# Kernel optimization log

Measured on AMD Instinct MI355X. Metric: run time of the kernel, lower is better.

Reference implementation:

```python
import jax, jax.numpy as jnp
import numpy as np

B, N, E = 8, 1024, 131072
DS, DT, D, HEADS = 768, 128, 256, 4
DH = D // HEADS  # 64, cross-attn head dim


def _gat(x, src, dst, lin_w, att_src, att_dst, bias, n):
    # PyG GATConv(heads=4, concat=False): per-head dim == out_channels == D
    xw = (x @ lin_w).reshape(n, HEADS, D)                  # [n,H,D]
    a_s = jnp.sum(xw * att_src, axis=-1)                   # [n,H]
    a_d = jnp.sum(xw * att_dst, axis=-1)                   # [n,H]
    alpha = jax.nn.leaky_relu(a_s[src] + a_d[dst], 0.2)    # [E',H]
    # softmax over incoming edges per destination node (self-loops guarantee non-empty segments)
    amax = jax.ops.segment_max(alpha, dst, num_segments=n)
    ex = jnp.exp(alpha - amax[dst])
    den = jax.ops.segment_sum(ex, dst, num_segments=n)
    w = ex / den[dst]                                      # [E',H]
    out = jax.ops.segment_sum(xw[src] * w[:, :, None], dst, num_segments=n)  # [n,H,D]
    return out.mean(axis=1) + bias                         # concat=False -> mean over heads


def _mha(q, kv, in_w, in_b, out_w, out_b):
    # torch nn.MultiheadAttention packed projections: in_w [3D,D], in_b [3D]
    qh = (q @ in_w[:D].T + in_b[:D]).reshape(B, N, HEADS, DH)
    kh = (kv @ in_w[D:2 * D].T + in_b[D:2 * D]).reshape(B, N, HEADS, DH)
    vh = (kv @ in_w[2 * D:].T + in_b[2 * D:]).reshape(B, N, HEADS, DH)
    s = jnp.einsum('bqhd,bkhd->bhqk', qh, kh) / np.float32(np.sqrt(DH))
    a = jax.nn.softmax(s, axis=-1)
    o = jnp.einsum('bhqk,bkhd->bqhd', a, vh).reshape(B, N, D)
    return o @ out_w.T + out_b


def _forward(structure_emb, text_emb, node_features, edit_emb_raw,
             ws, bs, wt, bt, we, be, wp, bp,
             g1_lin, g1_as, g1_ad, g1_b, g2_lin, g2_as, g2_ad, g2_b,
             mha_iw, mha_ib, mha_ow, mha_ob,
             cw1, cb1, cw2, cb2, aw1, ab1, aw2, ab2,
             edge_index, node_mask):
    maskf = node_mask.astype(jnp.float32)                  # [B,N]
    struct = structure_emb @ ws + bs                       # [B,N,D]
    textf = text_emb @ wt + bt                             # [B,D]
    editp = edit_emb_raw @ we + be                         # [B,D] (frozen-encoder CLS already precomputed)
    text_feat = jnp.broadcast_to(textf[:, None], (B, N, D))
    edit_feat = jnp.broadcast_to(editp[:, None], (B, N, D))
    combined = jnp.concatenate([struct, text_feat, edit_feat], axis=-1)  # [B,N,3D]
    node = (combined @ wp + bp) * maskf[..., None]
    x = node.reshape(B * N, D)
    edit_flat = edit_feat.reshape(B * N, D)
    n = B * N
    loops = jnp.arange(n, dtype=edge_index.dtype)          # GATConv default add_self_loops=True
    src = jnp.concatenate([edge_index[0], loops])
    dst = jnp.concatenate([edge_index[1], loops])
    x = jax.nn.relu(_gat(x + edit_flat, src, dst, g1_lin, g1_as, g1_ad, g1_b, n))
    x = jax.nn.relu(_gat(x + edit_flat, src, dst, g2_lin, g2_as, g2_ad, g2_b, n))
    node = x.reshape(B, N, D)
    # global attention over [text, edit] context tokens
    gte = jnp.stack([textf, editp], axis=1)                # [B,2,D]
    scores = jnp.einsum('bnd,bkd->bnk', node, gte) + (1.0 - maskf)[..., None] * -10000.0
    wglob = jax.nn.softmax(scores, axis=-1) @ gte          # [B,N,D]
    attn = _mha(node, text_feat, mha_iw, mha_ib, mha_ow, mha_ob)
    comb = node + wglob + attn
    coords = (jax.nn.relu(comb @ cw1 + cb1) @ cw2 + cb2) * maskf[..., None]   # [B,N,3]
    aa_logits = (jax.nn.relu(comb @ aw1 + ab1) @ aw2 + ab2) * maskf[..., None]  # [B,N,20]
    aa_probs = jax.nn.softmax(aa_logits, axis=-1) * maskf[..., None]
    return coords, aa_probs


def setup_inputs() -> dict:
    key = jax.random.key(0)
    ki = iter(jax.random.split(key, 48))
    def rn(shape, s=1.0):
        return jax.random.normal(next(ki), shape, jnp.float32) * s
    inp = {
        'structure_emb': rn((B, N, DS)),
        'text_emb': rn((B, DT)),
        'node_features': rn((B, N, D)),   # accepted by forward but unused (as in original)
        'edit_emb_raw': rn((B, DS)),
        'ws': rn((DS, D), 0.02), 'bs': rn((D,), 0.02),
        'wt': rn((DT, D), 0.02), 'bt': rn((D,), 0.02),
        'we': rn((DS, D), 0.02), 'be': rn((D,), 0.02),
        'wp': rn((3 * D, D), 0.02), 'bp': rn((D,), 0.02),
        'g1_lin': rn((D, HEADS * D), 0.02), 'g1_as': rn((HEADS, D), 0.02), 'g1_ad': rn((HEADS, D), 0.02), 'g1_b': rn((D,), 0.02),
        'g2_lin': rn((D, HEADS * D), 0.02), 'g2_as': rn((HEADS, D), 0.02), 'g2_ad': rn((HEADS, D), 0.02), 'g2_b': rn((D,), 0.02),
        'mha_iw': rn((3 * D, D), 0.02), 'mha_ib': rn((3 * D,), 0.02),
        'mha_ow': rn((D, D), 0.02), 'mha_ob': rn((D,), 0.02),
        'cw1': rn((D, D), 0.02), 'cb1': rn((D,), 0.02), 'cw2': rn((D, 3), 0.02), 'cb2': rn((3,), 0.02),
        'aw1': rn((D, D), 0.02), 'ab1': rn((D,), 0.02), 'aw2': rn((D, 20), 0.02), 'ab2': rn((20,), 0.02),
        'edge_index': jax.random.randint(next(ki), (2, E), 0, B * N, dtype=jnp.int32),
        'node_mask': jnp.ones((B, N), dtype=bool),
    }
    return inp


def reference(structure_emb, text_emb, node_features, edit_emb_raw,
              ws, bs, wt, bt, we, be, wp, bp,
              g1_lin, g1_as, g1_ad, g1_b, g2_lin, g2_as, g2_ad, g2_b,
              mha_iw, mha_ib, mha_ow, mha_ob,
              cw1, cb1, cw2, cb2, aw1, ab1, aw2, ab2,
              edge_index, node_mask):
    return _forward(structure_emb, text_emb, node_features, edit_emb_raw,
                    ws, bs, wt, bt, we, be, wp, bp,
                    g1_lin, g1_as, g1_ad, g1_b, g2_lin, g2_as, g2_ad, g2_b,
                    mha_iw, mha_ib, mha_ow, mha_ob,
                    cw1, cb1, cw2, cb2, aw1, ab1, aw2, ab2,
                    edge_index, node_mask)
```

## Files before the change

### kernel.cpp

```cpp
#include <hip/hip_runtime.h>
#include <hip/hip_bf16.h>

#define BB 8
#define NN 1024
#define BN 8192
#define DD 256
#define HEADS 4
#define HD 1024
#define DSS 768
#define DTT 128
#define NE 131072
#define NEP (NE + BN)
#define DEGCAP 256

typedef __hip_bfloat16 bf16;
typedef __attribute__((ext_vector_type(8))) short short8;
typedef __attribute__((ext_vector_type(4))) float floatx4;

__device__ __forceinline__ float toF(bf16 x){ return __bfloat162float(x); }
__device__ __forceinline__ void stC(float* p, float v){ *p = v; }
__device__ __forceinline__ void stC(bf16* p, float v){ *p = __float2bfloat16(v); }
__device__ __forceinline__ float bf_lo(unsigned u){ return __uint_as_float(u << 16); }
__device__ __forceinline__ float bf_hi(unsigned u){ return __uint_as_float(u & 0xffff0000u); }

__device__ __forceinline__ float wredsum(float v){
  #pragma unroll
  for (int off = 32; off; off >>= 1) v += __shfl_xor(v, off);
  return v;
}
__device__ __forceinline__ float wredmax(float v){
  #pragma unroll
  for (int off = 32; off; off >>= 1) v = fmaxf(v, __shfl_xor(v, off));
  return v;
}

__device__ __forceinline__ void dev_transpose(
    float tb[32][33], const float* __restrict__ src, bf16* __restrict__ dst,
    int R, int C, int bx, int by, int tid)
{
  int c0 = bx*32, r0 = by*32;
  int tr = tid >> 5, tc = tid & 31;
  #pragma unroll
  for (int i = 0; i < 4; i++)
    tb[tr + i*8][tc] = src[(size_t)(r0 + tr + i*8)*C + c0 + tc];
  __syncthreads();
  #pragma unroll
  for (int i = 0; i < 4; i++)
    dst[(size_t)(c0 + tr + i*8)*R + r0 + tc] = __float2bfloat16(tb[tc][tr + i*8]);
}

__global__ __launch_bounds__(256) void prep1(
    const float* __restrict__ text_emb, const float* __restrict__ edit_emb,
    const float* __restrict__ wt, const float* __restrict__ bt,
    const float* __restrict__ we, const float* __restrict__ be,
    float* __restrict__ textf, float* __restrict__ editp,
    const float* __restrict__ wsm, const float* __restrict__ wp, bf16* __restrict__ WfT,
    const float* __restrict__ semb, bf16* __restrict__ sembB,
    const float* __restrict__ g1_lin, bf16* __restrict__ g1T,
    const float* __restrict__ g2_lin, bf16* __restrict__ g2T,
    const float* __restrict__ cw1, const float* __restrict__ aw1, bf16* __restrict__ W2T,
    const float* __restrict__ cw2, const float* __restrict__ cb2,
    const float* __restrict__ aw2, const float* __restrict__ ab2,
    bf16* __restrict__ WdT, float* __restrict__ bias23,
    int* __restrict__ counts, int* __restrict__ fc, float* __restrict__ zz,
    const float* __restrict__ cb1, const float* __restrict__ ab1, float* __restrict__ bias2)
{
  __shared__ float tpose[32][33];
  __shared__ float red[2][4][64];
  int blk = blockIdx.x, tid = threadIdx.x;
  if (blk < 32) {
    int b = blk & 7, l = tid & 63, qq = tid >> 6;
    int d = (blk >> 3)*64 + l;
    float tf = 0.f;
    for (int k = qq*32; k < qq*32 + 32; k++) tf += text_emb[b*DTT + k] * wt[(size_t)k*DD + d];
    float ep = 0.f;
    for (int k = qq*192; k < qq*192 + 192; k++) ep += edit_emb[b*DSS + k] * we[(size_t)k*DD + d];
    red[0][qq][l] = tf; red[1][qq][l] = ep;
    __syncthreads();
    if (tid < 64) {
      int dd = (blk >> 3)*64 + tid;
      textf[b*DD + dd] = red[0][0][tid]+red[0][1][tid]+red[0][2][tid]+red[0][3][tid] + bt[dd];
      editp[b*DD + dd] = red[1][0][tid]+red[1][1][tid]+red[1][2][tid]+red[1][3][tid] + be[dd];
    }
  } else if (blk < 128) {
    int k0 = (blk - 32)*8, d = tid;
    float acc[8] = {};
    for (int j = 0; j < DD; j++) {
      float wv = wp[(size_t)j*DD + d];
      #pragma unroll
      for (int kk = 0; kk < 8; kk++) acc[kk] += wsm[(size_t)(k0 + kk)*DD + j] * wv;
    }
    #pragma unroll
    for (int kk = 0; kk < 8; kk++) WfT[(size_t)d*DSS + k0 + kk] = __float2bfloat16(acc[kk]);
  } else if (blk < 6272) {
    int i = ((blk - 128)*256 + tid)*4;
    float4 v = *(const float4*)(semb + i);
    bf16 t4[4] = {__float2bfloat16(v.x), __float2bfloat16(v.y),
                  __float2bfloat16(v.z), __float2bfloat16(v.w)};
    *(uint2*)(sembB + i) = *(uint2*)t4;
  } else if (blk < 6528) {
    int lo = blk - 6272; dev_transpose(tpose, g1_lin, g1T, DD, HD, lo & 31, lo >> 5, tid);
  } else if (blk < 6784) {
    int lo = blk - 6528; dev_transpose(tpose, g2_lin, g2T, DD, HD, lo & 31, lo >> 5, tid);
  } else if (blk < 6848) {
    int lo = blk - 6784; dev_transpose(tpose, cw1, W2T, DD, DD, lo & 7, lo >> 3, tid);
  } else if (blk < 6912) {
    int lo = blk - 6848; dev_transpose(tpose, aw1, W2T + 65536, DD, DD, lo & 7, lo >> 3, tid);
  } else if (blk < 7040) {
    int idx = (blk - 6912)*256 + tid;
    int n = idx >> 9, k = idx & 511;
    float v = 0.f;
    if (n < 3) { if (k < 256) v = cw2[(size_t)k*3 + n]; }
    else if (n < 23) { if (k >= 256) v = aw2[(size_t)(k - 256)*20 + (n - 3)]; }
    WdT[idx] = __float2bfloat16(v);
    if (idx < 64) bias23[idx] = idx < 3 ? cb2[idx] : (idx < 23 ? ab2[idx - 3] : 0.f);
  } else {
    int i = (blk - 7040)*256 + tid;
    counts[i] = 1; fc[i] = 0;
    float4 z = make_float4(0.f, 0.f, 0.f, 0.f);
    #pragma unroll
    for (int j = 0; j < 4; j++) ((float4*)zz)[i*4 + j] = z;
    if (i < 256) bias2[i] = cb1[i];
    else if (i < 512) bias2[i] = ab1[i - 256];
  }
}

__global__ __launch_bounds__(256) void prep2(
    const float* __restrict__ textf, const float* __restrict__ editp,
    const float* __restrict__ mha_iw, const float* __restrict__ mha_ib, float* __restrict__ vh,
    const float* __restrict__ bs, const float* __restrict__ wp, const float* __restrict__ bp,
    float* __restrict__ cvec,
    const int* __restrict__ ei, int* __restrict__ counts)
{
  __shared__ float red[4][64];
  int blk = blockIdx.x, tid = threadIdx.x;
  if (blk < 512) {
    int b = blk & 7, w = tid >> 6, l = tid & 63;
    int d = (blk >> 3)*4 + w;
    float p = 0.f;
    #pragma unroll
    for (int i = 0; i < 4; i++) p += textf[b*DD + l + 64*i] * mha_iw[(size_t)(512 + d)*DD + l + 64*i];
    p = wredsum(p);
    if (l == 0) vh[b*DD + d] = p + mha_ib[512 + d];
  } else if (blk < 544) {
    int lo = blk - 512;
    int b = lo & 7, l = tid & 63, qq = tid >> 6;
    int d = (lo >> 3)*64 + l;
    float cv = 0.f;
    for (int k = qq*64; k < qq*64 + 64; k++) cv += bs[k] * wp[(size_t)k*DD + d];
    for (int k = qq*64; k < qq*64 + 64; k++) cv += textf[b*DD + k] * wp[(size_t)(DD + k)*DD + d];
    for (int k = qq*64; k < qq*64 + 64; k++) cv += editp[b*DD + k] * wp[(size_t)(2*DD + k)*DD + d];
    red[qq][l] = cv;
    __syncthreads();
    if (tid < 64) {
      int dd = (lo >> 3)*64 + tid;
      cvec[b*DD + dd] = red[0][tid]+red[1][tid]+red[2][tid]+red[3][tid] + bp[dd] + editp[b*DD + dd];
    }
  } else {
    int e = (blk - 544)*256 + tid;
    if (e < NE) atomicAdd(&counts[ei[NE + e]], 1);
  }
}

__global__ __launch_bounds__(1024) void prep3(
    const float* __restrict__ vh, const float* __restrict__ mha_ow,
    const float* __restrict__ mha_ob, float* __restrict__ mhavec,
    const int* __restrict__ counts, int* __restrict__ offs)
{
  __shared__ int part[1024];
  int blk = blockIdx.x, t = threadIdx.x;
  if (blk < 128) {
    int b = blk >> 4, w16 = t >> 6, l = t & 63;
    int d = (blk & 15)*16 + w16;
    float p = 0.f;
    #pragma unroll
    for (int i = 0; i < 4; i++) p += vh[b*DD + l + 64*i] * mha_ow[(size_t)d*DD + l + 64*i];
    p = wredsum(p);
    if (l == 0) mhavec[b*DD + d] = p + mha_ob[d];
  } else {
    int local[8]; int sum = 0;
    #pragma unroll
    for (int i = 0; i < 8; i++) { local[i] = sum; sum += counts[t*8 + i]; }
    part[t] = sum;
    __syncthreads();
    for (int off = 1; off < 1024; off <<= 1) {
      int v = (t >= off) ? part[t - off] : 0;
      __syncthreads();
      part[t] += v;
      __syncthreads();
    }
    int base = (t == 0) ? 0 : part[t - 1];
    #pragma unroll
    for (int i = 0; i < 8; i++) offs[t*8 + i] = base + local[i];
    if (t == 1023) offs[BN] = part[1023];
  }
}

__global__ void csr_fill(const int* __restrict__ ei, const int* __restrict__ offs,
                         int* __restrict__ fc, int* __restrict__ csr)
{
  int idx = blockIdx.x*256 + threadIdx.x;
  if (idx < NE) {
    int sn = ei[idx], dn = ei[NE + idx];
    int p = offs[dn] + atomicAdd(&fc[dn], 1);
    csr[p] = sn;
  } else if (idx < NEP) {
    int i2 = idx - NE;
    int p = offs[i2] + atomicAdd(&fc[i2], 1);
    csr[p] = i2;
  }
}

template<typename TC>
__global__ __launch_bounds__(256) void gemm_mfma(
    const bf16* __restrict__ A, const bf16* __restrict__ Bt, TC* __restrict__ C,
    int M, int N, int K,
    const float* __restrict__ bias, const float* __restrict__ rowvec, int relu,
    const float* __restrict__ atts, const float* __restrict__ attd,
    float* __restrict__ as_out, float* __restrict__ ad_out)
{
  __shared__ __align__(16) bf16 Asl[64*72];
  __shared__ __align__(16) bf16 Bsl[64*72];
  int tid = threadIdx.x;
  int w = tid >> 6, lane = tid & 63;
  int q = lane >> 4, mn = lane & 15;
  int row0 = blockIdx.y*64, col0 = blockIdx.x*64;
  int sr = tid >> 3, sc = tid & 7;
  floatx4 acc[4];
  #pragma unroll
  for (int t = 0; t < 4; t++) acc[t] = (floatx4){0.f, 0.f, 0.f, 0.f};

  for (int k0 = 0; k0 < K; k0 += 64) {
    uint4 a0 = *(const uint4*)(A  + (size_t)(row0 + sr)*K      + k0 + sc*8);
    uint4 a1 = *(const uint4*)(A  + (size_t)(row0 + 32 + sr)*K + k0 + sc*8);
    uint4 b0 = *(const uint4*)(Bt + (size_t)(col0 + sr)*K      + k0 + sc*8);
    uint4 b1 = *(const uint4*)(Bt + (size_t)(col0 + 32 + sr)*K + k0 + sc*8);
    __syncthreads();
    *(uint4*)&Asl[sr*72 + sc*8]        = a0;
    *(uint4*)&Asl[(sr + 32)*72 + sc*8] = a1;
    *(uint4*)&Bsl[sr*72 + sc*8]        = b0;
    *(uint4*)&Bsl[(sr + 32)*72 + sc*8] = b1;
    __syncthreads();
    #pragma unroll
    for (int kk = 0; kk < 64; kk += 32) {
      short8 af = *(const short8*)&Asl[(w*16 + mn)*72 + kk + q*8];
      #pragma unroll
      for (int t = 0; t < 4; t++) {
        short8 bfr = *(const short8*)&Bsl[(t*16 + mn)*72 + kk + q*8];
        acc[t] = __builtin_amdgcn_mfma_f32_16x16x32_bf16(af, bfr, acc[t], 0, 0, 0);
      }
    }
  }
  if (as_out) {
    int h = col0 >> 8, cbase = col0 & 255;
    float ps[4] = {}, pd[4] = {};
    #pragma unroll
    for (int t = 0; t < 4; t++) {
      float av = atts[h*DD + cbase + t*16 + mn];
      float dv = attd[h*DD + cbase + t*16 + mn];
      #pragma unroll
      for (int rg = 0; rg < 4; rg++) {
        ps[rg] += acc[t][rg]*av;
        pd[rg] += acc[t][rg]*dv;
      }
    }
    #pragma unroll
    for (int rg = 0; rg < 4; rg++) {
      #pragma unroll
      for (int off = 1; off < 16; off <<= 1) {
        ps[rg] += __shfl_xor(ps[rg], off);
        pd[rg] += __shfl_xor(pd[rg], off);
      }
      if (mn == 0) {
        int r = row0 + w*16 + q*4 + rg;
        atomicAdd(&as_out[r*4 + h], ps[rg]);
        atomicAdd(&ad_out[r*4 + h], pd[rg]);
      }
    }
  }
  #pragma unroll
  for (int t = 0; t < 4; t++) {
    #pragma unroll
    for (int rg = 0; rg < 4; rg++) {
      int r = row0 + w*16 + q*4 + rg;
      int c = col0 + t*16 + mn;
      float v = acc[t][rg];
      if (bias)   v += bias[c];
      if (rowvec) v += rowvec[(size_t)(r >> 10)*N + c];
      if (relu)   v = fmaxf(v, 0.f);
      stC(&C[(size_t)r*N + c], v);
    }
  }
}

__global__ __launch_bounds__(256) void gemm_fin(
    const bf16* __restrict__ A, const bf16* __restrict__ Bt,
    const float* __restrict__ bias, float* __restrict__ out)
{
  __shared__ __align__(16) bf16 Asl[64*72];
  __shared__ __align__(16) bf16 Bsl[64*72];
  const int K = 512;
  int tid = threadIdx.x;
  int w = tid >> 6, lane = tid & 63;
  int q = lane >> 4, mn = lane & 15;
  int row0 = blockIdx.x*64;
  int sr = tid >> 3, sc = tid & 7;
  floatx4 acc[4];
  #pragma unroll
  for (int t = 0; t < 4; t++) acc[t] = (floatx4){0.f, 0.f, 0.f, 0.f};
  for (int k0 = 0; k0 < K; k0 += 64) {
    uint4 a0 = *(const uint4*)(A  + (size_t)(row0 + sr)*K      + k0 + sc*8);
    uint4 a1 = *(const uint4*)(A  + (size_t)(row0 + 32 + sr)*K + k0 + sc*8);
    uint4 b0 = *(const uint4*)(Bt + (size_t)sr*K      + k0 + sc*8);
    uint4 b1 = *(const uint4*)(Bt + (size_t)(32 + sr)*K + k0 + sc*8);
    __syncthreads();
    *(uint4*)&Asl[sr*72 + sc*8]        = a0;
    *(uint4*)&Asl[(sr + 32)*72 + sc*8] = a1;
    *(uint4*)&Bsl[sr*72 + sc*8]        = b0;
    *(uint4*)&Bsl[(sr + 32)*72 + sc*8] = b1;
    __syncthreads();
    #pragma unroll
    for (int kk = 0; kk < 64; kk += 32) {
      short8 af = *(const short8*)&Asl[(w*16 + mn)*72 + kk + q*8];
      #pragma unroll
      for (int t = 0; t < 4; t++) {
        short8 bfr = *(const short8*)&Bsl[(t*16 + mn)*72 + kk + q*8];
        acc[t] = __builtin_amdgcn_mfma_f32_16x16x32_bf16(af, bfr, acc[t], 0, 0, 0);
      }
    }
  }
  #pragma unroll
  for (int rg = 0; rg < 4; rg++) {
    int r = row0 + w*16 + q*4 + rg;
    float mx = -1e30f;
    #pragma unroll
    for (int t = 0; t < 4; t++) {
      int c = t*16 + mn;
      float val = acc[t][rg] + bias[c];
      if (c >= 3 && c < 23) mx = fmaxf(mx, val);
    }
    #pragma unroll
    for (int off = 1; off < 16; off <<= 1) mx = fmaxf(mx, __shfl_xor(mx, off));
    float sum = 0.f;
    #pragma unroll
    for (int t = 0; t < 4; t++) {
      int c = t*16 + mn;
      float val = acc[t][rg] + bias[c];
      if (c >= 3 && c < 23) sum += expf(val - mx);
    }
    #pragma unroll
    for (int off = 1; off < 16; off <<= 1) sum += __shfl_xor(sum, off);
    float inv = 1.f / sum;
    #pragma unroll
    for (int t = 0; t < 2; t++) {
      int c = t*16 + mn;
      float val = acc[t][rg] + bias[c];
      if (c < 3) out[(size_t)r*3 + c] = val;
      else if (c < 23) out[24576 + (size_t)r*20 + (c - 3)] = expf(val - mx)*inv;
    }
  }
}

__global__ __launch_bounds__(256) void gat_aggregate(
    const bf16* __restrict__ xw, const float* __restrict__ a_s, const float* __restrict__ a_d,
    const int* __restrict__ offs, const int* __restrict__ csr,
    const float* __restrict__ bias, const float* __restrict__ editadd,
    const float* __restrict__ ctext, const float* __restrict__ cedit,
    const float* __restrict__ cmha,
    bf16* __restrict__ xout)
{
  int i = blockIdx.x, t = threadIdx.x;
  int h = t >> 6, l = t & 63;
  int beg = offs[i], end = offs[i + 1], deg = end - beg;
  __shared__ float sacc[HD];
  __shared__ float sal[4][DEGCAP];
  __shared__ int   scsr[DEGCAP];
  float adh = a_d[i*4 + h];
  float mloc = -1e30f;
  for (int idx = l; idx < deg; idx += 64) {
    int sn = csr[beg + idx];
    if (h == 0 && idx < DEGCAP) scsr[idx] = sn;
    float al = a_s[sn*4 + h] + adh;
    al = al > 0.f ? al : 0.2f*al;
    if (idx < DEGCAP) sal[h][idx] = al;
    mloc = fmaxf(mloc, al);
  }
  float mh = wredmax(mloc);
  float sloc = 0.f;
  for (int idx = l; idx < deg; idx += 64) {
    float al;
    if (idx < DEGCAP) al = sal[h][idx];
    else {
      int sn = csr[beg + idx];
      al = a_s[sn*4 + h] + adh;
      al = al > 0.f ? al : 0.2f*al;
    }
    float wv = expf(al - mh);
    if (idx < DEGCAP) sal[h][idx] = wv;
    sloc += wv;
  }
  float inv = 1.f / wredsum(sloc);
  __syncthreads();
  const bf16* xbase = xw + h*DD + l*4;
  float acc0 = 0.f, acc1 = 0.f, acc2 = 0.f, acc3 = 0.f;
  int cached = deg < DEGCAP ? deg : DEGCAP;
  for (int idx = 0; idx < cached; idx++) {
    int sn = scsr[idx];
    float wv = sal[h][idx];
    uint2 u = *(const uint2*)(xbase + (size_t)sn*HD);
    acc0 += wv*bf_lo(u.x); acc1 += wv*bf_hi(u.x);
    acc2 += wv*bf_lo(u.y); acc3 += wv*bf_hi(u.y);
  }
  for (int idx = cached; idx < deg; idx++) {
    int sn = csr[beg + idx];
    float al = a_s[sn*4 + h] + adh;
    al = al > 0.f ? al : 0.2f*al;
    float wv = expf(al - mh);
    uint2 u = *(const uint2*)(xbase + (size_t)sn*HD);
    acc0 += wv*bf_lo(u.x); acc1 += wv*bf_hi(u.x);
    acc2 += wv*bf_lo(u.y); acc3 += wv*bf_hi(u.y);
  }
  sacc[h*DD + l*4 + 0] = acc0*inv;
  sacc[h*DD + l*4 + 1] = acc1*inv;
  sacc[h*DD + l*4 + 2] = acc2*inv;
  sacc[h*DD + l*4 + 3] = acc3*inv;
  __syncthreads();
  if (t < 64) {
    int b = i >> 10;
    float v[4], tx[4], ex[4];
    #pragma unroll
    for (int j = 0; j < 4; j++) {
      int d = t*4 + j;
      float x = 0.25f*(sacc[d] + sacc[DD + d] + sacc[2*DD + d] + sacc[3*DD + d]) + bias[d];
      v[j] = fmaxf(x, 0.f);
    }
    if (cmha) {
      float s0 = 0.f, s1 = 0.f;
      #pragma unroll
      for (int j = 0; j < 4; j++) {
        int d = t*4 + j;
        tx[j] = ctext[b*DD + d]; ex[j] = cedit[b*DD + d];
        s0 += v[j]*tx[j]; s1 += v[j]*ex[j];
      }
      s0 = wredsum(s0); s1 = wredsum(s1);
      float mm = fmaxf(s0, s1);
      float e0 = expf(s0 - mm), e1 = expf(s1 - mm);
      float inv2 = 1.f / (e0 + e1);
      float p0 = e0*inv2, p1 = e1*inv2;
      #pragma unroll
      for (int j = 0; j < 4; j++) {
        int d = t*4 + j;
        xout[(size_t)i*DD + d] = __float2bfloat16(v[j] + p0*tx[j] + p1*ex[j] + cmha[b*DD + d]);
      }
    } else {
      #pragma unroll
      for (int j = 0; j < 4; j++) {
        int d = t*4 + j;
        float x = v[j];
        if (editadd) x += editadd[b*DD + d];
        xout[(size_t)i*DD + d] = __float2bfloat16(x);
      }
    }
  }
}

extern "C" void kernel_launch(void* const* d_in, const int* in_sizes, int n_in,
                              void* d_out, int out_size, void* d_ws, size_t ws_size,
                              hipStream_t stream)
{
  (void)in_sizes; (void)n_in; (void)out_size; (void)ws_size;
  const float* structure_emb = (const float*)d_in[0];
  const float* text_emb      = (const float*)d_in[1];
  const float* edit_emb      = (const float*)d_in[3];
  const float* ws_w    = (const float*)d_in[4];
  const float* bs_b    = (const float*)d_in[5];
  const float* wt_w    = (const float*)d_in[6];
  const float* bt_b    = (const float*)d_in[7];
  const float* we_w    = (const float*)d_in[8];
  const float* be_b    = (const float*)d_in[9];
  const float* wp_w    = (const float*)d_in[10];
  const float* bp_b    = (const float*)d_in[11];
  const float* g1_lin  = (const float*)d_in[12];
  const float* g1_as   = (const float*)d_in[13];
  const float* g1_ad   = (const float*)d_in[14];
  const float* g1_b    = (const float*)d_in[15];
  const float* g2_lin  = (const float*)d_in[16];
  const float* g2_as   = (const float*)d_in[17];
  const float* g2_ad   = (const float*)d_in[18];
  const float* g2_b    = (const float*)d_in[19];
  const float* mha_iw  = (const float*)d_in[20];
  const float* mha_ib  = (const float*)d_in[21];
  const float* mha_ow  = (const float*)d_in[22];
  const float* mha_ob  = (const float*)d_in[23];
  const float* cw1     = (const float*)d_in[24];
  const float* cb1     = (const float*)d_in[25];
  const float* cw2     = (const float*)d_in[26];
  const float* cb2     = (const float*)d_in[27];
  const float* aw1     = (const float*)d_in[28];
  const float* ab1     = (const float*)d_in[29];
  const float* aw2     = (const float*)d_in[30];
  const float* ab2     = (const float*)d_in[31];
  const int*  edge_index = (const int*)d_in[32];
  float* out = (float*)d_out;

  char* p = (char*)d_ws;
  bf16*  sembB = (bf16*)p;
  bf16*  xwb   = (bf16*)p;
  bf16*  h1b   = (bf16*)p;
  p += 16777216;
  bf16* bufB = (bf16*)p; p += 4194304;
  bf16* g1T  = (bf16*)p; p += 524288;
  bf16* g2T  = (bf16*)p; p += 524288;
  bf16* W2T  = (bf16*)p; p += 262144;
  bf16* WfT  = (bf16*)p; p += 393216;
  bf16* WdT  = (bf16*)p; p += 65536;
  float* textf  = (float*)p; p += 8192;
  float* editp  = (float*)p; p += 8192;
  float* vhws   = (float*)p; p += 8192;
  float* mhavec = (float*)p; p += 8192;
  float* cvec   = (float*)p; p += 8192;
  float* bias2  = (float*)p; p += 2048;
  float* bias23 = (float*)p; p += 256;
  float* a_s1   = (float*)p; p += 131072;
  float* a_d1   = (float*)p; p += 131072;
  float* a_s2   = (float*)p; p += 131072;
  float* a_d2   = (float*)p; p += 131072;
  int* counts = (int*)p; p += 32768;
  int* offs   = (int*)p; p += 32784;
  int* fc     = (int*)p; p += 32768;
  int* csr    = (int*)p; p += NEP*4;

  prep1<<<7072, 256, 0, stream>>>(
      text_emb, edit_emb, wt_w, bt_b, we_w, be_b, textf, editp,
      ws_w, wp_w, WfT, structure_emb, sembB,
      g1_lin, g1T, g2_lin, g2T, cw1, aw1, W2T,
      cw2, cb2, aw2, ab2, WdT, bias23,
      counts, fc, a_s1, cb1, ab1, bias2);
  prep2<<<1056, 256, 0, stream>>>(
      textf, editp, mha_iw, mha_ib, vhws, bs_b, wp_w, bp_b, cvec,
      edge_index, counts);
  prep3<<<129, 1024, 0, stream>>>(vhws, mha_ow, mha_ob, mhavec, counts, offs);
  csr_fill<<<(NEP + 255)/256, 256, 0, stream>>>(edge_index, offs, fc, csr);

  gemm_mfma<bf16><<<dim3(DD/64, BN/64), 256, 0, stream>>>(
      sembB, WfT, bufB, BN, DD, DSS, nullptr, cvec, 0,
      nullptr, nullptr, nullptr, nullptr);

  gemm_mfma<bf16><<<dim3(HD/64, BN/64), 256, 0, stream>>>(
      bufB, g1T, xwb, BN, HD, DD, nullptr, nullptr, 0,
      g1_as, g1_ad, a_s1, a_d1);
  gat_aggregate<<<BN, 256, 0, stream>>>(xwb, a_s1, a_d1, offs, csr, g1_b, editp,
                                        nullptr, nullptr, nullptr, bufB);

  gemm_mfma<bf16><<<dim3(HD/64, BN/64), 256, 0, stream>>>(
      bufB, g2T, xwb, BN, HD, DD, nullptr, nullptr, 0,
      g2_as, g2_ad, a_s2, a_d2);
  gat_aggregate<<<BN, 256, 0, stream>>>(xwb, a_s2, a_d2, offs, csr, g2_b, nullptr,
                                        textf, editp, mhavec, bufB);

  gemm_mfma<bf16><<<dim3(512/64, BN/64), 256, 0, stream>>>(
      bufB, W2T, h1b, BN, 512, DD, bias2, nullptr, 1,
      nullptr, nullptr, nullptr, nullptr);

  gemm_fin<<<BN/64, 256, 0, stream>>>(h1b, WdT, bias23, out);
}
```

Before: 342.1 us.

## Use 128x128 MFMA tiles for GAT and MLP GEMMs; widen GAT gather loads

```diff
diff --git a/kernel.cpp b/kernel.cpp
--- a/kernel.cpp
+++ b/kernel.cpp
@@ -211,13 +211,9 @@
   }
 }
 
-template<typename TC>
-__global__ __launch_bounds__(256) void gemm_mfma(
-    const bf16* __restrict__ A, const bf16* __restrict__ Bt, TC* __restrict__ C,
-    int M, int N, int K,
-    const float* __restrict__ bias, const float* __restrict__ rowvec, int relu,
-    const float* __restrict__ atts, const float* __restrict__ attd,
-    float* __restrict__ as_out, float* __restrict__ ad_out)
+__global__ __launch_bounds__(256) void gemm_mfma64(
+    const bf16* __restrict__ A, const bf16* __restrict__ Bt, bf16* __restrict__ C,
+    int M, int N, int K, const float* __restrict__ rowvec)
 {
   __shared__ __align__(16) bf16 Asl[64*72];
   __shared__ __align__(16) bf16 Bsl[64*72];
@@ -229,7 +225,6 @@
   floatx4 acc[4];
   #pragma unroll
   for (int t = 0; t < 4; t++) acc[t] = (floatx4){0.f, 0.f, 0.f, 0.f};
-
   for (int k0 = 0; k0 < K; k0 += 64) {
     uint4 a0 = *(const uint4*)(A  + (size_t)(row0 + sr)*K      + k0 + sc*8);
     uint4 a1 = *(const uint4*)(A  + (size_t)(row0 + 32 + sr)*K + k0 + sc*8);
@@ -251,33 +246,6 @@
       }
     }
   }
-  if (as_out) {
-    int h = col0 >> 8, cbase = col0 & 255;
-    float ps[4] = {}, pd[4] = {};
-    #pragma unroll
-    for (int t = 0; t < 4; t++) {
-      float av = atts[h*DD + cbase + t*16 + mn];
-      float dv = attd[h*DD + cbase + t*16 + mn];
-      #pragma unroll
-      for (int rg = 0; rg < 4; rg++) {
-        ps[rg] += acc[t][rg]*av;
-        pd[rg] += acc[t][rg]*dv;
-      }
-    }
-    #pragma unroll
-    for (int rg = 0; rg < 4; rg++) {
-      #pragma unroll
-      for (int off = 1; off < 16; off <<= 1) {
-        ps[rg] += __shfl_xor(ps[rg], off);
-        pd[rg] += __shfl_xor(pd[rg], off);
-      }
-      if (mn == 0) {
-        int r = row0 + w*16 + q*4 + rg;
-        atomicAdd(&as_out[r*4 + h], ps[rg]);
-        atomicAdd(&ad_out[r*4 + h], pd[rg]);
-      }
-    }
-  }
   #pragma unroll
   for (int t = 0; t < 4; t++) {
     #pragma unroll
@@ -285,10 +253,107 @@
       int r = row0 + w*16 + q*4 + rg;
       int c = col0 + t*16 + mn;
       float v = acc[t][rg];
-      if (bias)   v += bias[c];
       if (rowvec) v += rowvec[(size_t)(r >> 10)*N + c];
-      if (relu)   v = fmaxf(v, 0.f);
-      stC(&C[(size_t)r*N + c], v);
+      C[(size_t)r*N + c] = __float2bfloat16(v);
+    }
+  }
+}
+
+template<typename TC>
+__global__ __launch_bounds__(256) void gemm_mfma128(
+    const bf16* __restrict__ A, const bf16* __restrict__ Bt, TC* __restrict__ C,
+    int M, int N, int K,
+    const float* __restrict__ bias, int relu,
+    const float* __restrict__ atts, const float* __restrict__ attd,
+    float* __restrict__ as_out, float* __restrict__ ad_out)
+{
+  __shared__ __align__(16) bf16 Asl[128*72];
+  __shared__ __align__(16) bf16 Bsl[128*72];
+  int tid = threadIdx.x;
+  int w = tid >> 6, lane = tid & 63;
+  int q = lane >> 4, mn = lane & 15;
+  int wr = w >> 1, wc = w & 1;
+  int row0 = blockIdx.y*128, col0 = blockIdx.x*128;
+  int sr = tid >> 3, sc = tid & 7;
+  floatx4 acc[4][4];
+  #pragma unroll
+  for (int tm = 0; tm < 4; tm++)
+    #pragma unroll
+    for (int tn = 0; tn < 4; tn++) acc[tm][tn] = (floatx4){0.f, 0.f, 0.f, 0.f};
+
+  for (int k0 = 0; k0 < K; k0 += 64) {
+    uint4 av[4], bv[4];
+    #pragma unroll
+    for (int i = 0; i < 4; i++) {
+      av[i] = *(const uint4*)(A  + (size_t)(row0 + sr + i*32)*K + k0 + sc*8);
+      bv[i] = *(const uint4*)(Bt + (size_t)(col0 + sr + i*32)*K + k0 + sc*8);
+    }
+    __syncthreads();
+    #pragma unroll
+    for (int i = 0; i < 4; i++) {
+      *(uint4*)&Asl[(sr + i*32)*72 + sc*8] = av[i];
+      *(uint4*)&Bsl[(sr + i*32)*72 + sc*8] = bv[i];
+    }
+    __syncthreads();
+    #pragma unroll
+    for (int kk = 0; kk < 64; kk += 32) {
+      short8 af[4], bfr[4];
+      #pragma unroll
+      for (int tm = 0; tm < 4; tm++)
+        af[tm] = *(const short8*)&Asl[(wr*64 + tm*16 + mn)*72 + kk + q*8];
+      #pragma unroll
+      for (int tn = 0; tn < 4; tn++)
+        bfr[tn] = *(const short8*)&Bsl[(wc*64 + tn*16 + mn)*72 + kk + q*8];
+      #pragma unroll
+      for (int tm = 0; tm < 4; tm++)
+        #pragma unroll
+        for (int tn = 0; tn < 4; tn++)
+          acc[tm][tn] = __builtin_amdgcn_mfma_f32_16x16x32_bf16(af[tm], bfr[tn], acc[tm][tn], 0, 0, 0);
+    }
+  }
+  if (as_out) {
+    int h = (col0 + wc*64) >> 8, cb = (col0 + wc*64) & 255;
+    #pragma unroll
+    for (int tm = 0; tm < 4; tm++) {
+      float ps[4] = {}, pd[4] = {};
+      #pragma unroll
+      for (int tn = 0; tn < 4; tn++) {
+        float avv = atts[h*DD + cb + tn*16 + mn];
+        float dvv = attd[h*DD + cb + tn*16 + mn];
+        #pragma unroll
+        for (int rg = 0; rg < 4; rg++) {
+          ps[rg] += acc[tm][tn][rg]*avv;
+          pd[rg] += acc[tm][tn][rg]*dvv;
+        }
+      }
+      #pragma unroll
+      for (int rg = 0; rg < 4; rg++) {
+        #pragma unroll
+        for (int off = 1; off < 16; off <<= 1) {
+          ps[rg] += __shfl_xor(ps[rg], off);
+          pd[rg] += __shfl_xor(pd[rg], off);
+        }
+        if (mn == 0) {
+          int r = row0 + wr*64 + tm*16 + q*4 + rg;
+          atomicAdd(&as_out[r*4 + h], ps[rg]);
+          atomicAdd(&ad_out[r*4 + h], pd[rg]);
+        }
+      }
+    }
+  }
+  #pragma unroll
+  for (int tm = 0; tm < 4; tm++) {
+    #pragma unroll
+    for (int tn = 0; tn < 4; tn++) {
+      #pragma unroll
+      for (int rg = 0; rg < 4; rg++) {
+        int r = row0 + wr*64 + tm*16 + q*4 + rg;
+        int c = col0 + wc*64 + tn*16 + mn;
+        float v = acc[tm][tn][rg];
+        if (bias) v += bias[c];
+        if (relu) v = fmaxf(v, 0.f);
+        stC(&C[(size_t)r*N + c], v);
+      }
     }
   }
 }
@@ -401,29 +466,39 @@
   }
   float inv = 1.f / wredsum(sloc);
   __syncthreads();
-  const bf16* xbase = xw + h*DD + l*4;
-  float acc0 = 0.f, acc1 = 0.f, acc2 = 0.f, acc3 = 0.f;
+  int sub = l >> 5, lc = l & 31;
+  const bf16* xbase = xw + h*DD + lc*8;
+  float a0=0.f,a1=0.f,a2=0.f,a3=0.f,a4=0.f,a5=0.f,a6=0.f,a7=0.f;
   int cached = deg < DEGCAP ? deg : DEGCAP;
-  for (int idx = 0; idx < cached; idx++) {
+  for (int idx = sub; idx < cached; idx += 2) {
     int sn = scsr[idx];
     float wv = sal[h][idx];
-    uint2 u = *(const uint2*)(xbase + (size_t)sn*HD);
-    acc0 += wv*bf_lo(u.x); acc1 += wv*bf_hi(u.x);
-    acc2 += wv*bf_lo(u.y); acc3 += wv*bf_hi(u.y);
-  }
-  for (int idx = cached; idx < deg; idx++) {
+    uint4 u = *(const uint4*)(xbase + (size_t)sn*HD);
+    a0 += wv*bf_lo(u.x); a1 += wv*bf_hi(u.x);
+    a2 += wv*bf_lo(u.y); a3 += wv*bf_hi(u.y);
+    a4 += wv*bf_lo(u.z); a5 += wv*bf_hi(u.z);
+    a6 += wv*bf_lo(u.w); a7 += wv*bf_hi(u.w);
+  }
+  for (int idx = cached + sub; idx < deg; idx += 2) {
     int sn = csr[beg + idx];
     float al = a_s[sn*4 + h] + adh;
     al = al > 0.f ? al : 0.2f*al;
     float wv = expf(al - mh);
-    uint2 u = *(const uint2*)(xbase + (size_t)sn*HD);
-    acc0 += wv*bf_lo(u.x); acc1 += wv*bf_hi(u.x);
-    acc2 += wv*bf_lo(u.y); acc3 += wv*bf_hi(u.y);
-  }
-  sacc[h*DD + l*4 + 0] = acc0*inv;
-  sacc[h*DD + l*4 + 1] = acc1*inv;
-  sacc[h*DD + l*4 + 2] = acc2*inv;
-  sacc[h*DD + l*4 + 3] = acc3*inv;
+    uint4 u = *(const uint4*)(xbase + (size_t)sn*HD);
+    a0 += wv*bf_lo(u.x); a1 += wv*bf_hi(u.x);
+    a2 += wv*bf_lo(u.y); a3 += wv*bf_hi(u.y);
+    a4 += wv*bf_lo(u.z); a5 += wv*bf_hi(u.z);
+    a6 += wv*bf_lo(u.w); a7 += wv*bf_hi(u.w);
+  }
+  a0 += __shfl_xor(a0, 32); a1 += __shfl_xor(a1, 32);
+  a2 += __shfl_xor(a2, 32); a3 += __shfl_xor(a3, 32);
+  a4 += __shfl_xor(a4, 32); a5 += __shfl_xor(a5, 32);
+  a6 += __shfl_xor(a6, 32); a7 += __shfl_xor(a7, 32);
+  if (sub == 0) {
+    float* sp = &sacc[h*DD + lc*8];
+    sp[0]=a0*inv; sp[1]=a1*inv; sp[2]=a2*inv; sp[3]=a3*inv;
+    sp[4]=a4*inv; sp[5]=a5*inv; sp[6]=a6*inv; sp[7]=a7*inv;
+  }
   __syncthreads();
   if (t < 64) {
     int b = i >> 10;
@@ -542,24 +617,23 @@
   prep3<<<129, 1024, 0, stream>>>(vhws, mha_ow, mha_ob, mhavec, counts, offs);
   csr_fill<<<(NEP + 255)/256, 256, 0, stream>>>(edge_index, offs, fc, csr);
 
-  gemm_mfma<bf16><<<dim3(DD/64, BN/64), 256, 0, stream>>>(
-      sembB, WfT, bufB, BN, DD, DSS, nullptr, cvec, 0,
-      nullptr, nullptr, nullptr, nullptr);
-
-  gemm_mfma<bf16><<<dim3(HD/64, BN/64), 256, 0, stream>>>(
-      bufB, g1T, xwb, BN, HD, DD, nullptr, nullptr, 0,
+  gemm_mfma64<<<dim3(DD/64, BN/64), 256, 0, stream>>>(
+      sembB, WfT, bufB, BN, DD, DSS, cvec);
+
+  gemm_mfma128<bf16><<<dim3(HD/128, BN/128), 256, 0, stream>>>(
+      bufB, g1T, xwb, BN, HD, DD, nullptr, 0,
       g1_as, g1_ad, a_s1, a_d1);
   gat_aggregate<<<BN, 256, 0, stream>>>(xwb, a_s1, a_d1, offs, csr, g1_b, editp,
                                         nullptr, nullptr, nullptr, bufB);
 
-  gemm_mfma<bf16><<<dim3(HD/64, BN/64), 256, 0, stream>>>(
-      bufB, g2T, xwb, BN, HD, DD, nullptr, nullptr, 0,
+  gemm_mfma128<bf16><<<dim3(HD/128, BN/128), 256, 0, stream>>>(
+      bufB, g2T, xwb, BN, HD, DD, nullptr, 0,
       g2_as, g2_ad, a_s2, a_d2);
   gat_aggregate<<<BN, 256, 0, stream>>>(xwb, a_s2, a_d2, offs, csr, g2_b, nullptr,
                                         textf, editp, mhavec, bufB);
 
-  gemm_mfma<bf16><<<dim3(512/64, BN/64), 256, 0, stream>>>(
-      bufB, W2T, h1b, BN, 512, DD, bias2, nullptr, 1,
+  gemm_mfma128<bf16><<<dim3(512/128, BN/128), 256, 0, stream>>>(
+      bufB, W2T, h1b, BN, 512, DD, bias2, 1,
       nullptr, nullptr, nullptr, nullptr);
 
   gemm_fin<<<BN/64, 256, 0, stream>>>(h1b, WdT, bias23, out);
```

After: 403.9 us. 1.18x slower.
